# Performance work log

Measured on AMD Instinct MI355X. Metric: run time of the kernel, lower is better.

## Reference

```python
import jax, jax.numpy as jnp
import numpy as np

B, S, D = 16, 300, 768   # batch, hubert frames, embedding_dim
K = 512                  # vq codebook size
V = 5000                 # vocab size
H = 8                    # attention heads
NL = 4                   # encoder/decoder layers
L = 50                   # label length
EPS = 1e-5


def layer_norm(x, g, b):
    m = jnp.mean(x, axis=-1, keepdims=True)
    v = jnp.var(x, axis=-1, keepdims=True)
    return (x - m) * jax.lax.rsqrt(v + EPS) * g + b


def mha(q_in, kv_in, Wqkv, bqkv, Wo, bo, bias=None):
    # PyTorch nn.MultiheadAttention math (packed in_proj), batch_first
    Dm = q_in.shape[-1]
    hd = Dm // H
    Wq, Wk, Wv = jnp.split(Wqkv, 3, axis=0)
    bq, bk, bv = jnp.split(bqkv, 3, axis=0)
    q = (q_in @ Wq.T + bq).reshape(q_in.shape[0], -1, H, hd)
    k = (kv_in @ Wk.T + bk).reshape(kv_in.shape[0], -1, H, hd)
    v = (kv_in @ Wv.T + bv).reshape(kv_in.shape[0], -1, H, hd)
    scores = jnp.einsum('bthd,bshd->bhts', q, k) / jnp.sqrt(jnp.float32(hd))
    if bias is not None:
        scores = scores + bias
    a = jax.nn.softmax(scores, axis=-1)
    o = jnp.einsum('bhts,bshd->bthd', a, v).reshape(q_in.shape[0], -1, Dm)
    return o @ Wo.T + bo


def setup_inputs() -> dict:
    key = jax.random.key(0)
    ks = iter(jax.random.split(key, 64))
    f32 = jnp.float32
    def rn(shape, s=0.02):
        return jax.random.normal(next(ks), shape, f32) * s
    d = {}
    d['features'] = jax.random.normal(next(ks), (B, S, D), f32)
    d['labels'] = jax.random.randint(next(ks), (B, L), 1, V, jnp.int32)
    d['codebook'] = jax.random.normal(next(ks), (K, D), f32)   # normal_() init
    d['emb_layer'] = jax.random.normal(next(ks), (K, D), f32)  # nn.Embedding N(0,1)
    d['tok_emb'] = jax.random.normal(next(ks), (V, D), f32)
    d['fc_W'] = rn((V, D)); d['fc_b'] = jnp.zeros((V,), f32)
    for p in ['enc', 'dec_s', 'dec_c']:
        d[p + 'Wqkv' if p != 'enc' else 'enc_Wqkv'] = rn((NL, 3 * D, D))
    # rebuild cleanly with explicit names
    d['enc_Wqkv'] = rn((NL, 3 * D, D)); d['enc_bqkv'] = jnp.zeros((NL, 3 * D), f32)
    d['enc_Wo'] = rn((NL, D, D)); d['enc_bo'] = jnp.zeros((NL, D), f32)
    d['enc_ln1g'] = jnp.ones((NL, D), f32); d['enc_ln1b'] = jnp.zeros((NL, D), f32)
    d['enc_W1'] = rn((NL, 1536, D)); d['enc_b1'] = jnp.zeros((NL, 1536), f32)
    d['enc_W2'] = rn((NL, D, 1536)); d['enc_b2'] = jnp.zeros((NL, D), f32)
    d['enc_ln2g'] = jnp.ones((NL, D), f32); d['enc_ln2b'] = jnp.zeros((NL, D), f32)
    d['dec_sWqkv'] = rn((NL, 3 * D, D)); d['dec_sbqkv'] = jnp.zeros((NL, 3 * D), f32)
    d['dec_sWo'] = rn((NL, D, D)); d['dec_sbo'] = jnp.zeros((NL, D), f32)
    d['dec_cWqkv'] = rn((NL, 3 * D, D)); d['dec_cbqkv'] = jnp.zeros((NL, 3 * D), f32)
    d['dec_cWo'] = rn((NL, D, D)); d['dec_cbo'] = jnp.zeros((NL, D), f32)
    d['dec_ln1g'] = jnp.ones((NL, D), f32); d['dec_ln1b'] = jnp.zeros((NL, D), f32)
    d['dec_ln2g'] = jnp.ones((NL, D), f32); d['dec_ln2b'] = jnp.zeros((NL, D), f32)
    d['dec_ln3g'] = jnp.ones((NL, D), f32); d['dec_ln3b'] = jnp.zeros((NL, D), f32)
    d['dec_W1'] = rn((NL, 1536, D)); d['dec_b1'] = jnp.zeros((NL, 1536), f32)
    d['dec_W2'] = rn((NL, D, 1536)); d['dec_b2'] = jnp.zeros((NL, D), f32)
    return d


def forward(features, labels, codebook, emb_layer, tok_emb, fc_W, fc_b,
            enc_Wqkv, enc_bqkv, enc_Wo, enc_bo, enc_ln1g, enc_ln1b,
            enc_W1, enc_b1, enc_W2, enc_b2, enc_ln2g, enc_ln2b,
            dec_sWqkv, dec_sbqkv, dec_sWo, dec_sbo,
            dec_cWqkv, dec_cbqkv, dec_cWo, dec_cbo,
            dec_ln1g, dec_ln1b, dec_ln2g, dec_ln2b, dec_ln3g, dec_ln3b,
            dec_W1, dec_b1, dec_W2, dec_b2):
    # ---- VQ: pairwise distances + argmin + codebook gather ----
    x = features.reshape(-1, D)                                  # [N, D]
    dist = (jnp.sum(x * x, 1, keepdims=True)
            + jnp.sum(codebook * codebook, 1)
            - 2.0 * x @ codebook.T)                              # [N, K]
    idx = jnp.argmin(dist, axis=1)                               # [N]
    quantized = codebook[idx]                                    # one-hot @ codebook == gather
    # commitment loss (quantized is detached in e_latent_loss)
    vq_loss = 0.25 * jnp.mean((jax.lax.stop_gradient(quantized) - x) ** 2)
    # ---- encoder over embedding_layer lookup of the VQ indices ----
    h = emb_layer[idx].reshape(B, S, D)
    for i in range(NL):
        h = layer_norm(h + mha(h, h, enc_Wqkv[i], enc_bqkv[i], enc_Wo[i], enc_bo[i]),
                       enc_ln1g[i], enc_ln1b[i])
        ff = jax.nn.relu(h @ enc_W1[i].T + enc_b1[i]) @ enc_W2[i].T + enc_b2[i]
        h = layer_norm(h + ff, enc_ln2g[i], enc_ln2b[i])
    memory = h
    # ---- decoder (teacher forcing) ----
    dec_in = tok_emb[labels][:, :-1, :]                          # [B, L-1, D]
    target = labels[:, 1:]                                       # [B, L-1]
    T = L - 1
    causal = jnp.triu(jnp.ones((T, T), bool), 1)                 # tgt_mask
    kpm = (target == 0)[:, None, None, :]                        # tgt_key_padding_mask
    bias = jnp.where(causal[None, None] | kpm, jnp.float32(-1e9), jnp.float32(0.0))
    y = dec_in
    for i in range(NL):
        y = layer_norm(y + mha(y, y, dec_sWqkv[i], dec_sbqkv[i], dec_sWo[i], dec_sbo[i], bias),
                       dec_ln1g[i], dec_ln1b[i])
        y = layer_norm(y + mha(y, memory, dec_cWqkv[i], dec_cbqkv[i], dec_cWo[i], dec_cbo[i]),
                       dec_ln2g[i], dec_ln2b[i])
        ff = jax.nn.relu(y @ dec_W1[i].T + dec_b1[i]) @ dec_W2[i].T + dec_b2[i]
        y = layer_norm(y + ff, dec_ln3g[i], dec_ln3b[i])
    logits = y @ fc_W.T + fc_b                                   # [B, L-1, V]
    return logits, vq_loss, target


def reference(features, labels, codebook, emb_layer, tok_emb, fc_W, fc_b,
              enc_Wqkv, enc_bqkv, enc_Wo, enc_bo, enc_ln1g, enc_ln1b,
              enc_W1, enc_b1, enc_W2, enc_b2, enc_ln2g, enc_ln2b,
              dec_sWqkv, dec_sbqkv, dec_sWo, dec_sbo,
              dec_cWqkv, dec_cbqkv, dec_cWo, dec_cbo,
              dec_ln1g, dec_ln1b, dec_ln2g, dec_ln2b, dec_ln3g, dec_ln3b,
              dec_W1, dec_b1, dec_W2, dec_b2):
    return forward(features, labels, codebook, emb_layer, tok_emb, fc_W, fc_b,
                   enc_Wqkv, enc_bqkv, enc_Wo, enc_bo, enc_ln1g, enc_ln1b,
                   enc_W1, enc_b1, enc_W2, enc_b2, enc_ln2g, enc_ln2b,
                   dec_sWqkv, dec_sbqkv, dec_sWo, dec_sbo,
                   dec_cWqkv, dec_cbqkv, dec_cWo, dec_cbo,
                   dec_ln1g, dec_ln1b, dec_ln2g, dec_ln2b, dec_ln3g, dec_ln3b,
                   dec_W1, dec_b1, dec_W2, dec_b2)
```

## Files before the change

### kernel.cpp

```cpp
#include <hip/hip_runtime.h>
#include <hip/hip_bf16.h>

#define Bz   16
#define Sz   300
#define Dz   768
#define Kc   512
#define Vz   5000
#define Hh   8
#define HD   96
#define Lz   50
#define Tz   49
#define NTOK 4800
#define NDTOK 784

typedef short bf16x8 __attribute__((ext_vector_type(8)));
typedef float f32x4  __attribute__((ext_vector_type(4)));
typedef unsigned short us8 __attribute__((ext_vector_type(8)));

__device__ __forceinline__ unsigned short f2b(float f) {
    unsigned u = __float_as_uint(f);
    unsigned r = (u + 0x7fffu + ((u >> 16) & 1u)) >> 16;
    return (unsigned short)r;
}

__device__ __forceinline__ void glds16(const unsigned short* g, unsigned short* l) {
    __builtin_amdgcn_global_load_lds(
        (const __attribute__((address_space(1))) void*)g,
        (__attribute__((address_space(3))) void*)l, 16, 0, 0);
}

__global__ __launch_bounds__(256) void gemm_bf16_kernel(
    const unsigned short* __restrict__ A,
    const unsigned short* __restrict__ Bw,
    float* __restrict__ Cf,
    unsigned short* __restrict__ Cb,
    int ldc,
    const float* __restrict__ bias,
    const float* __restrict__ resid, int ldr,
    int relu, int M, int N, int Kd)
{
    __shared__ unsigned short As[128 * 32];
    __shared__ unsigned short Bs[128 * 32];
    const int tid  = threadIdx.x;
    const int wave = tid >> 6, lane = tid & 63;
    const int row0 = blockIdx.y * 128, col0 = blockIdx.x * 128;

    const int c0 = wave * 2;
    const int srow = lane >> 2;
    const int skcol = (lane & 3) * 8;
    int rA0 = row0 + c0 * 16 + srow;        if (rA0 > M - 1) rA0 = M - 1;
    int rA1 = row0 + (c0 + 1) * 16 + srow;  if (rA1 > M - 1) rA1 = M - 1;
    int rB0 = col0 + c0 * 16 + srow;        if (rB0 > N - 1) rB0 = N - 1;
    int rB1 = col0 + (c0 + 1) * 16 + srow;  if (rB1 > N - 1) rB1 = N - 1;
    const unsigned short* pA0 = A + (size_t)rA0 * Kd + skcol;
    const unsigned short* pA1 = A + (size_t)rA1 * Kd + skcol;
    const unsigned short* pB0 = Bw + (size_t)rB0 * Kd + skcol;
    const unsigned short* pB1 = Bw + (size_t)rB1 * Kd + skcol;
    unsigned short* lA0 = &As[c0 * 512];
    unsigned short* lA1 = &As[(c0 + 1) * 512];
    unsigned short* lB0 = &Bs[c0 * 512];
    unsigned short* lB1 = &Bs[(c0 + 1) * 512];

    const int wr = (wave >> 1) * 64, wc = (wave & 1) * 64;
    const int fr = lane & 15;
    const int kq = (lane >> 4) * 8;

    f32x4 acc[4][4];
    const f32x4 zero = { 0.f, 0.f, 0.f, 0.f };
#pragma unroll
    for (int i = 0; i < 4; ++i)
#pragma unroll
        for (int j = 0; j < 4; ++j) acc[i][j] = zero;

    for (int k0 = 0; k0 < Kd; k0 += 32) {
        __syncthreads();
        glds16(pA0 + k0, lA0);
        glds16(pA1 + k0, lA1);
        glds16(pB0 + k0, lB0);
        glds16(pB1 + k0, lB1);
        __syncthreads();

        bf16x8 af[4], bfr[4];
#pragma unroll
        for (int i = 0; i < 4; ++i)
            af[i] = *(const bf16x8*)(const void*)(&As[(wr + i * 16 + fr) * 32 + kq]);
#pragma unroll
        for (int j = 0; j < 4; ++j)
            bfr[j] = *(const bf16x8*)(const void*)(&Bs[(wc + j * 16 + fr) * 32 + kq]);
#pragma unroll
        for (int i = 0; i < 4; ++i)
#pragma unroll
            for (int j = 0; j < 4; ++j)
                acc[i][j] = __builtin_amdgcn_mfma_f32_16x16x32_bf16(
                    af[i], bfr[j], acc[i][j], 0, 0, 0);
    }

    const int rbase = row0 + wr + ((lane >> 4) << 2);
    const int cbase = col0 + wc + (lane & 15);
#pragma unroll
    for (int i = 0; i < 4; ++i) {
#pragma unroll
        for (int r = 0; r < 4; ++r) {
            int row = rbase + i * 16 + r;
            if (row >= M) continue;
#pragma unroll
            for (int j = 0; j < 4; ++j) {
                int col = cbase + j * 16;
                if (col >= N) continue;
                float v = acc[i][j][r];
                if (bias)  v += bias[col];
                if (resid) v += resid[(size_t)row * ldr + col];
                if (relu)  v = fmaxf(v, 0.f);
                if (Cf) Cf[(size_t)row * ldc + col] = v;
                if (Cb) Cb[(size_t)row * ldc + col] = f2b(v);
            }
        }
    }
}

__global__ __launch_bounds__(256) void gemm_bf16_64_kernel(
    const unsigned short* __restrict__ A,
    const unsigned short* __restrict__ Bw,
    float* __restrict__ Cf, unsigned short* __restrict__ Cb, int ldc,
    const float* __restrict__ bias,
    const float* __restrict__ resid, int ldr,
    int relu, int M, int N, int Kd)
{
    __shared__ unsigned short As[64 * 32];
    __shared__ unsigned short Bs[64 * 32];
    const int tid = threadIdx.x, wave = tid >> 6, lane = tid & 63;
    const int row0 = blockIdx.y * 64, col0 = blockIdx.x * 64;
    const int fr = lane & 15, quad = lane >> 4;

    const int sr = lane >> 2;
    const int sc = (lane & 3) * 8;
    int ra = row0 + wave * 16 + sr;  if (ra > M - 1) ra = M - 1;
    int rb = col0 + wave * 16 + sr;  if (rb > N - 1) rb = N - 1;
    const unsigned short* pA = A + (size_t)ra * Kd + sc;
    const unsigned short* pB = Bw + (size_t)rb * Kd + sc;
    unsigned short* lA = &As[wave * 512];
    unsigned short* lB = &Bs[wave * 512];

    f32x4 acc[4];
    const f32x4 zero = { 0.f, 0.f, 0.f, 0.f };
#pragma unroll
    for (int j = 0; j < 4; ++j) acc[j] = zero;

    for (int k0 = 0; k0 < Kd; k0 += 32) {
        __syncthreads();
        glds16(pA + k0, lA);
        glds16(pB + k0, lB);
        __syncthreads();
        bf16x8 a = *(const bf16x8*)(const void*)(&As[(wave * 16 + fr) * 32 + quad * 8]);
#pragma unroll
        for (int j = 0; j < 4; ++j) {
            bf16x8 b = *(const bf16x8*)(const void*)(&Bs[(j * 16 + fr) * 32 + quad * 8]);
            acc[j] = __builtin_amdgcn_mfma_f32_16x16x32_bf16(a, b, acc[j], 0, 0, 0);
        }
    }

    const int rbase = row0 + wave * 16 + quad * 4;
    const int cbase = col0 + fr;
#pragma unroll
    for (int r = 0; r < 4; ++r) {
        int row = rbase + r;
        if (row >= M) continue;
#pragma unroll
        for (int j = 0; j < 4; ++j) {
            int col = cbase + j * 16;
            if (col >= N) continue;
            float v = acc[j][r];
            if (bias)  v += bias[col];
            if (resid) v += resid[(size_t)row * ldr + col];
            if (relu)  v = fmaxf(v, 0.f);
            if (Cf) Cf[(size_t)row * ldc + col] = v;
            if (Cb) Cb[(size_t)row * ldc + col] = f2b(v);
        }
    }
}

__global__ __launch_bounds__(256) void vq_gemm_kernel(
    const float* __restrict__ A,
    const float* __restrict__ Bw,
    float* __restrict__ C)
{
    __shared__ float As[16][64];
    __shared__ float Bs[16][64];
    const int tid = threadIdx.x;
    const int row0 = blockIdx.y * 64, col0 = blockIdx.x * 64;
    const int tx = tid & 15, ty = tid >> 4;
    const int lm = tid >> 2, lk = (tid & 3) * 4;

    float acc[4][4];
#pragma unroll
    for (int i = 0; i < 4; ++i)
#pragma unroll
        for (int j = 0; j < 4; ++j) acc[i][j] = 0.f;

    const float* Ap = A + (size_t)(row0 + lm) * Dz + lk;
    const float* Bp = Bw + (size_t)(col0 + lm) * Dz + lk;

    for (int k0 = 0; k0 < Dz; k0 += 16) {
        float4 av = *(const float4*)(Ap + k0);
        float4 bv = *(const float4*)(Bp + k0);
        __syncthreads();
        As[lk + 0][lm] = av.x; As[lk + 1][lm] = av.y;
        As[lk + 2][lm] = av.z; As[lk + 3][lm] = av.w;
        Bs[lk + 0][lm] = bv.x; Bs[lk + 1][lm] = bv.y;
        Bs[lk + 2][lm] = bv.z; Bs[lk + 3][lm] = bv.w;
        __syncthreads();
#pragma unroll
        for (int kk = 0; kk < 16; ++kk) {
            float4 a4 = *(const float4*)&As[kk][ty * 4];
            float4 b4 = *(const float4*)&Bs[kk][tx * 4];
            float a[4] = { a4.x, a4.y, a4.z, a4.w };
            float b[4] = { b4.x, b4.y, b4.z, b4.w };
#pragma unroll
            for (int i = 0; i < 4; ++i)
#pragma unroll
                for (int j = 0; j < 4; ++j)
                    acc[i][j] = fmaf(a[i], b[j], acc[i][j]);
        }
    }

#pragma unroll
    for (int i = 0; i < 4; ++i)
#pragma unroll
        for (int j = 0; j < 4; ++j)
            C[(size_t)(row0 + ty * 4 + i) * Kc + col0 + tx * 4 + j] = acc[i][j];
}

#define SC_LD 324
#define P_LD  328
#define QK_LD 104
#define VT_LD 40

__global__ __launch_bounds__(256) void attn_mfma_kernel(
    const unsigned short* __restrict__ Qp, int qld, int qoff,
    const unsigned short* __restrict__ Kp, int kld, int koff,
    const unsigned short* __restrict__ Vp, int vld, int voff,
    unsigned short* __restrict__ Op,
    int Sq, int Sk, float scale, int causal,
    const int* __restrict__ lab)
{
    const int qt = blockIdx.x, h = blockIdx.y, b = blockIdx.z;
    const int q0 = qt * 32;
    __shared__ __align__(16) unsigned short Qs[32 * QK_LD];
    __shared__ __align__(16) unsigned short KVu[96 * VT_LD];
    __shared__ __align__(16) float Sc[32 * SC_LD];
    __shared__ __align__(16) unsigned short Pb[32 * P_LD];
    __shared__ float rinv[32];

    const int tid = threadIdx.x;
    const int wave = tid >> 6, lane = tid & 63;
    const int fr = lane & 15, quad = lane >> 4;
    const int nst = (Sk + 31) / 32;
    const int cmax = nst * 32;

    for (int e = tid; e < 384; e += 256) {
        int r = e / 12, c8 = (e % 12) * 8;
        int gq = q0 + r; if (gq >= Sq) gq = Sq - 1;
        us8 v = *(const us8*)(Qp + (size_t)(b * Sq + gq) * qld + qoff + h * HD + c8);
        *(us8*)(&Qs[r * QK_LD + c8]) = v;
    }

    const int mi = wave & 1;
    const int sw = wave >> 1;
    for (int it = 0; it < nst; ++it) {
        int s0 = it * 32;
        __syncthreads();
        for (int e = tid; e < 384; e += 256) {
            int r = e / 12, c8 = (e % 12) * 8;
            int gk = s0 + r; if (gk >= Sk) gk = Sk - 1;
            us8 v = *(const us8*)(Kp + (size_t)(b * Sk + gk) * kld + koff + h * HD + c8);
            *(us8*)(&KVu[r * QK_LD + c8]) = v;
        }
        __syncthreads();
        f32x4 acc = { 0.f, 0.f, 0.f, 0.f };
#pragma unroll
        for (int kk = 0; kk < 3; ++kk) {
            bf16x8 a = *(const bf16x8*)(const void*)(&Qs[(mi * 16 + fr) * QK_LD + kk * 32 + quad * 8]);
            bf16x8 bb = *(const bf16x8*)(const void*)(&KVu[(sw * 16 + fr) * QK_LD + kk * 32 + quad * 8]);
            acc = __builtin_amdgcn_mfma_f32_16x16x32_bf16(a, bb, acc, 0, 0, 0);
        }
        float* dst = &Sc[(mi * 16 + quad * 4) * SC_LD + s0 + sw * 16 + fr];
#pragma unroll
        for (int r = 0; r < 4; ++r) dst[r * SC_LD] = acc[r];
    }
    __syncthreads();

    {
        const int r = tid >> 3, sub = tid & 7;
        const int gq = q0 + r;
        float mx = -3e38f;
        for (int c = sub; c < cmax; c += 8) {
            float v = Sc[r * SC_LD + c];
            bool ok = (c < Sk);
            if (causal && c > gq) ok = false;
            if (ok && lab && lab[b * Lz + c + 1] == 0) ok = false;
            v = ok ? v * scale : -3e38f;
            Sc[r * SC_LD + c] = v;
            mx = fmaxf(mx, v);
        }
#pragma unroll
        for (int off = 4; off > 0; off >>= 1) mx = fmaxf(mx, __shfl_xor(mx, off));
        float sum = 0.f;
        for (int c = sub; c < cmax; c += 8) {
            float p = __expf(Sc[r * SC_LD + c] - mx);
            sum += p;
            Pb[r * P_LD + c] = f2b(p);
        }
#pragma unroll
        for (int off = 4; off > 0; off >>= 1) sum += __shfl_xor(sum, off);
        if (sub == 0) rinv[r] = 1.f / sum;
    }

    const int nbase = (wave >> 1) * 3;
    f32x4 oacc[3];
#pragma unroll
    for (int t = 0; t < 3; ++t) oacc[t] = (f32x4){ 0.f, 0.f, 0.f, 0.f };

    for (int it = 0; it < nst; ++it) {
        int s0 = it * 32;
        __syncthreads();
        for (int e = tid; e < 384; e += 256) {
            int r = e / 12, c8 = (e % 12) * 8;
            int gk = s0 + r; if (gk >= Sk) gk = Sk - 1;
            us8 v = *(const us8*)(Vp + (size_t)(b * Sk + gk) * vld + voff + h * HD + c8);
            const int f = ((c8 >> 3) & 3) << 3;
            const int rx = r ^ f;
#pragma unroll
            for (int j = 0; j < 8; ++j)
                KVu[(c8 + j) * VT_LD + rx] = v[j];
        }
        __syncthreads();
        bf16x8 a = *(const bf16x8*)(const void*)(&Pb[(mi * 16 + fr) * P_LD + s0 + quad * 8]);
#pragma unroll
        for (int t = 0; t < 3; ++t) {
            const int dcol = (nbase + t) * 16 + fr;
            const int f2 = ((dcol >> 3) & 3) << 3;
            bf16x8 bv = *(const bf16x8*)(const void*)(&KVu[dcol * VT_LD + ((quad * 8) ^ f2)]);
            oacc[t] = __builtin_amdgcn_mfma_f32_16x16x32_bf16(a, bv, oacc[t], 0, 0, 0);
        }
    }

#pragma unroll
    for (int t = 0; t < 3; ++t) {
#pragma unroll
        for (int r = 0; r < 4; ++r) {
            int lrow = mi * 16 + quad * 4 + r;
            int grow = q0 + lrow;
            if (grow >= Sq) continue;
            int col = h * HD + (nbase + t) * 16 + fr;
            Op[(size_t)(b * Sq + grow) * Dz + col] = f2b(oacc[t][r] * rinv[lrow]);
        }
    }
}

__global__ __launch_bounds__(256) void ln_kernel(
    const float* __restrict__ X, float* __restrict__ Y,
    unsigned short* __restrict__ Ybf,
    const float* __restrict__ g, const float* __restrict__ bb)
{
    const int n = blockIdx.x;
    const int tid = threadIdx.x;
    const float* x = X + (size_t)n * Dz;
    float v0 = x[tid], v1 = x[tid + 256], v2 = x[tid + 512];
    float s = v0 + v1 + v2;
    float q = v0 * v0 + v1 * v1 + v2 * v2;
#pragma unroll
    for (int off = 32; off > 0; off >>= 1) {
        s += __shfl_down(s, off);
        q += __shfl_down(q, off);
    }
    __shared__ float sbuf[4], qbuf[4];
    __shared__ float mv[2];
    int wid = tid >> 6;
    if ((tid & 63) == 0) { sbuf[wid] = s; qbuf[wid] = q; }
    __syncthreads();
    if (tid == 0) {
        float ts = sbuf[0] + sbuf[1] + sbuf[2] + sbuf[3];
        float tq = qbuf[0] + qbuf[1] + qbuf[2] + qbuf[3];
        float mean = ts * (1.f / 768.f);
        float var = tq * (1.f / 768.f) - mean * mean;
        mv[0] = mean;
        mv[1] = rsqrtf(var + 1e-5f);
    }
    __syncthreads();
    float mean = mv[0], inv = mv[1];
    float* y = Y + (size_t)n * Dz;
    float r0 = (v0 - mean) * inv * g[tid]       + bb[tid];
    float r1 = (v1 - mean) * inv * g[tid + 256] + bb[tid + 256];
    float r2 = (v2 - mean) * inv * g[tid + 512] + bb[tid + 512];
    y[tid] = r0; y[tid + 256] = r1; y[tid + 512] = r2;
    if (Ybf) {
        unsigned short* yb = Ybf + (size_t)n * Dz;
        yb[tid] = f2b(r0); yb[tid + 256] = f2b(r1); yb[tid + 512] = f2b(r2);
    }
}

__global__ __launch_bounds__(256) void sumsq_kernel(
    const float* __restrict__ cb, float* __restrict__ out)
{
    const int c = blockIdx.x, tid = threadIdx.x;
    const float* x = cb + (size_t)c * Dz;
    float v0 = x[tid], v1 = x[tid + 256], v2 = x[tid + 512];
    float q = v0 * v0 + v1 * v1 + v2 * v2;
#pragma unroll
    for (int off = 32; off > 0; off >>= 1) q += __shfl_down(q, off);
    __shared__ float qbuf[4];
    int wid = tid >> 6;
    if ((tid & 63) == 0) qbuf[wid] = q;
    __syncthreads();
    if (tid == 0) out[c] = qbuf[0] + qbuf[1] + qbuf[2] + qbuf[3];
}

__global__ __launch_bounds__(256) void vq_post_kernel(
    const float* __restrict__ dots, const float* __restrict__ sumc2,
    const float* __restrict__ feats, const float* __restrict__ codebook,
    const float* __restrict__ emb, float* __restrict__ H,
    unsigned short* __restrict__ Hbf,
    float* __restrict__ loss)
{
    const int n = blockIdx.x, tid = threadIdx.x;
    float best = 3.4e38f; int bi = 0;
    for (int c = tid; c < Kc; c += 256) {
        float dct = sumc2[c] - 2.f * dots[(size_t)n * Kc + c];
        if (dct < best) { best = dct; bi = c; }
    }
#pragma unroll
    for (int off = 32; off > 0; off >>= 1) {
        float ov = __shfl_down(best, off);
        int   oi = __shfl_down(bi, off);
        if (ov < best || (ov == best && oi < bi)) { best = ov; bi = oi; }
    }
    __shared__ float vb[4]; __shared__ int ib[4];
    __shared__ int bidx;
    int wid = tid >> 6;
    if ((tid & 63) == 0) { vb[wid] = best; ib[wid] = bi; }
    __syncthreads();
    if (tid == 0) {
        float v = vb[0]; int i = ib[0];
        for (int w = 1; w < 4; ++w)
            if (vb[w] < v || (vb[w] == v && ib[w] < i)) { v = vb[w]; i = ib[w]; }
        bidx = i;
    }
    __syncthreads();
    const int c = bidx;
    float part = 0.f;
    for (int d = tid; d < Dz; d += 256) {
        float xv = feats[(size_t)n * Dz + d];
        float cv = codebook[(size_t)c * Dz + d];
        float df = cv - xv;
        part += df * df;
        float ev = emb[(size_t)c * Dz + d];
        H[(size_t)n * Dz + d] = ev;
        Hbf[(size_t)n * Dz + d] = f2b(ev);
    }
#pragma unroll
    for (int off = 32; off > 0; off >>= 1) part += __shfl_down(part, off);
    __shared__ float pb[4];
    if ((tid & 63) == 0) pb[wid] = part;
    __syncthreads();
    if (tid == 0) atomicAdd(loss, pb[0] + pb[1] + pb[2] + pb[3]);
}

__global__ __launch_bounds__(256) void dec_embed_kernel(
    const int* __restrict__ labels, const float* __restrict__ tok,
    float* __restrict__ Y, unsigned short* __restrict__ Ybf,
    float* __restrict__ tgt)
{
    const int t = blockIdx.x;
    const int b = t / Tz, pos = t % Tz;
    const int lab = labels[b * Lz + pos];
    const int tid = threadIdx.x;
    const float* src = tok + (size_t)lab * Dz;
    float* dst = Y + (size_t)t * Dz;
    unsigned short* dbf = Ybf + (size_t)t * Dz;
    float a = src[tid], b1 = src[tid + 256], c = src[tid + 512];
    dst[tid] = a; dst[tid + 256] = b1; dst[tid + 512] = c;
    dbf[tid] = f2b(a); dbf[tid + 256] = f2b(b1); dbf[tid + 512] = f2b(c);
    if (tid == 0) tgt[t] = (float)labels[b * Lz + pos + 1];
}

__global__ void zero_loss_kernel(float* loss) { *loss = 0.f; }

__global__ void finalize_kernel(const float* loss, float* out)
{
    out[0] = loss[0] * (0.25f / (float)(NTOK * Dz));
}

__global__ __launch_bounds__(256) void conv6_kernel(
    const float* p0, int n0, const float* p1, int n1,
    const float* p2, int n2, const float* p3, int n3,
    const float* p4, int n4, const float* p5, int n5,
    unsigned short* __restrict__ dst)
{
    const int total = n0 + n1 + n2 + n3 + n4 + n5;
    for (int i = blockIdx.x * blockDim.x + threadIdx.x; i < total;
         i += gridDim.x * blockDim.x) {
        int j = i; const float* p;
        if (j < n0) { p = p0; }
        else { j -= n0;
            if (j < n1) { p = p1; }
            else { j -= n1;
                if (j < n2) { p = p2; }
                else { j -= n2;
                    if (j < n3) { p = p3; }
                    else { j -= n3;
                        if (j < n4) { p = p4; }
                        else { j -= n4; p = p5; }
                    }
                }
            }
        }
        dst[i] = f2b(p[j]);
    }
}

extern "C" void kernel_launch(void* const* d_in, const int* in_sizes, int n_in,
                              void* d_out, int out_size, void* d_ws, size_t ws_size,
                              hipStream_t stream)
{
    bool sig = (n_in > 8 && in_sizes[8] == 9216);
    int I_eWqkv, I_ebqkv, I_eWo, I_ebo, I_eln1g, I_eln1b, I_eW1, I_eb1, I_eW2, I_eb2,
        I_eln2g, I_eln2b, I_sWqkv, I_sbqkv, I_sWo, I_sbo, I_cWqkv, I_cbqkv, I_cWo,
        I_cbo, I_dln1g, I_dln1b, I_dln2g, I_dln2b, I_dln3g, I_dln3b, I_dW1, I_db1,
        I_dW2, I_db2;
    if (sig) {
        I_eWqkv = 7; I_ebqkv = 8; I_eWo = 9; I_ebo = 10; I_eln1g = 11; I_eln1b = 12;
        I_eW1 = 13; I_eb1 = 14; I_eW2 = 15; I_eb2 = 16; I_eln2g = 17; I_eln2b = 18;
        I_sWqkv = 19; I_sbqkv = 20; I_sWo = 21; I_sbo = 22;
        I_cWqkv = 23; I_cbqkv = 24; I_cWo = 25; I_cbo = 26;
        I_dln1g = 27; I_dln1b = 28; I_dln2g = 29; I_dln2b = 30; I_dln3g = 31; I_dln3b = 32;
        I_dW1 = 33; I_db1 = 34; I_dW2 = 35; I_db2 = 36;
    } else {
        I_eWqkv = 7; I_sWqkv = 8; I_cWqkv = 9;
        I_ebqkv = 10; I_eWo = 11; I_ebo = 12; I_eln1g = 13; I_eln1b = 14;
        I_eW1 = 15; I_eb1 = 16; I_eW2 = 17; I_eb2 = 18; I_eln2g = 19; I_eln2b = 20;
        I_sbqkv = 21; I_sWo = 22; I_sbo = 23;
        I_cbqkv = 24; I_cWo = 25; I_cbo = 26;
        I_dln1g = 27; I_dln1b = 28; I_dln2g = 29; I_dln2b = 30; I_dln3g = 31; I_dln3b = 32;
        I_dW1 = 33; I_db1 = 34; I_dW2 = 35; I_db2 = 36;
    }

    const float* feats = (const float*)d_in[0];
    const int*   labels = (const int*)d_in[1];
    const float* cb    = (const float*)d_in[2];
    const float* emb   = (const float*)d_in[3];
    const float* tok   = (const float*)d_in[4];
    const float* fcW   = (const float*)d_in[5];
    const float* fcb   = (const float*)d_in[6];
    const float* eWqkv = (const float*)d_in[I_eWqkv];
    const float* ebqkv = (const float*)d_in[I_ebqkv];
    const float* eWo   = (const float*)d_in[I_eWo];
    const float* ebo   = (const float*)d_in[I_ebo];
    const float* eln1g = (const float*)d_in[I_eln1g];
    const float* eln1b = (const float*)d_in[I_eln1b];
    const float* eW1   = (const float*)d_in[I_eW1];
    const float* eb1   = (const float*)d_in[I_eb1];
    const float* eW2   = (const float*)d_in[I_eW2];
    const float* eb2   = (const float*)d_in[I_eb2];
    const float* eln2g = (const float*)d_in[I_eln2g];
    const float* eln2b = (const float*)d_in[I_eln2b];
    const float* sWqkv = (const float*)d_in[I_sWqkv];
    const float* sbqkv = (const float*)d_in[I_sbqkv];
    const float* sWo   = (const float*)d_in[I_sWo];
    const float* sbo   = (const float*)d_in[I_sbo];
    const float* cWqkv = (const float*)d_in[I_cWqkv];
    const float* cbqkv = (const float*)d_in[I_cbqkv];
    const float* cWo   = (const float*)d_in[I_cWo];
    const float* cbo   = (const float*)d_in[I_cbo];
    const float* dln1g = (const float*)d_in[I_dln1g];
    const float* dln1b = (const float*)d_in[I_dln1b];
    const float* dln2g = (const float*)d_in[I_dln2g];
    const float* dln2b = (const float*)d_in[I_dln2b];
    const float* dln3g = (const float*)d_in[I_dln3g];
    const float* dln3b = (const float*)d_in[I_dln3b];
    const float* dW1   = (const float*)d_in[I_dW1];
    const float* db1   = (const float*)d_in[I_db1];
    const float* dW2   = (const float*)d_in[I_dW2];
    const float* db2   = (const float*)d_in[I_db2];

    float* ws    = (float*)d_ws;
    float* sumc2 = ws;
    float* loss  = ws + 512;
    float* Hb    = ws + 1024;
    float* T1    = ws + 3687424;
    float* dots  = ws + 7373824;
    float* Yb    = T1;
    float* T1d   = T1 + 602112;

    unsigned short* bfbase = (unsigned short*)(ws + 9831424);
    unsigned short* Hb_bf  = bfbase;
    unsigned short* ATT_bf = bfbase + 3686400;
    unsigned short* FF_bf  = bfbase + 7372800;
    unsigned short* Yb_bf  = bfbase + 14745600;
    unsigned short* Wbuf   = bfbase + 15347712;
    unsigned short* QKV_bf = bfbase + 22425600;
    unsigned short* QKVd_bf = QKV_bf;
    unsigned short* Qc_bf   = QKV_bf + 1806336;
    unsigned short* CKV_bf  = QKV_bf + 2408448;

    float* outF = (float*)d_out;

    auto gemmb = [&](const unsigned short* A, const unsigned short* W,
                     float* Cf, unsigned short* Cb, int ldc,
                     const float* bias, const float* resid, int ldr,
                     int relu, int M, int N, int Kd) {
        dim3 g((N + 127) / 128, (M + 127) / 128);
        gemm_bf16_kernel<<<g, 256, 0, stream>>>(A, W, Cf, Cb, ldc, bias, resid, ldr,
                                                relu, M, N, Kd);
    };
    auto gemmb64 = [&](const unsigned short* A, const unsigned short* W,
                       float* Cf, unsigned short* Cb, int ldc,
                       const float* bias, const float* resid, int ldr,
                       int relu, int M, int N, int Kd) {
        dim3 g((N + 63) / 64, (M + 63) / 64);
        gemm_bf16_64_kernel<<<g, 256, 0, stream>>>(A, W, Cf, Cb, ldc, bias, resid, ldr,
                                                   relu, M, N, Kd);
    };

    const float scale = 0.1020620726159658f;
    const float* Z = nullptr;

    zero_loss_kernel<<<1, 1, 0, stream>>>(loss);
    sumsq_kernel<<<Kc, 256, 0, stream>>>(cb, sumc2);
    vq_gemm_kernel<<<dim3(8, 75), 256, 0, stream>>>(feats, cb, dots);
    vq_post_kernel<<<NTOK, 256, 0, stream>>>(dots, sumc2, feats, cb, emb, Hb, Hb_bf, loss);
    finalize_kernel<<<1, 1, 0, stream>>>(loss, outF + 3920000);

    const int W_QKV = 2304 * 768, W_O = 768 * 768, W_F1 = 1536 * 768, W_F2 = 768 * 1536;
    for (int i = 0; i < 4; ++i) {
        conv6_kernel<<<1024, 256, 0, stream>>>(
            eWqkv + (size_t)i * W_QKV, W_QKV,
            eWo   + (size_t)i * W_O,   W_O,
            eW1   + (size_t)i * W_F1,  W_F1,
            eW2   + (size_t)i * W_F2,  W_F2,
            Z, 0, Z, 0, Wbuf);
        unsigned short* bWqkv = Wbuf;
        unsigned short* bWo   = Wbuf + W_QKV;
        unsigned short* bW1   = Wbuf + W_QKV + W_O;
        unsigned short* bW2   = Wbuf + W_QKV + W_O + W_F1;

        gemmb(Hb_bf, bWqkv, nullptr, QKV_bf, 2304, ebqkv + i * 2304, Z, 0, 0, NTOK, 2304, Dz);
        attn_mfma_kernel<<<dim3(10, Hh, Bz), 256, 0, stream>>>(
            QKV_bf, 2304, 0, QKV_bf, 2304, 768, QKV_bf, 2304, 1536, ATT_bf,
            Sz, Sz, scale, 0, nullptr);
        gemmb(ATT_bf, bWo, T1, nullptr, Dz, ebo + i * Dz, Hb, Dz, 0, NTOK, Dz, Dz);
        ln_kernel<<<NTOK, 256, 0, stream>>>(T1, Hb, Hb_bf, eln1g + i * Dz, eln1b + i * Dz);
        gemmb(Hb_bf, bW1, nullptr, FF_bf, 1536, eb1 + i * 1536, Z, 0, 1, NTOK, 1536, Dz);
        gemmb(FF_bf, bW2, T1, nullptr, Dz, eb2 + i * Dz, Hb, Dz, 0, NTOK, Dz, 1536);
        ln_kernel<<<NTOK, 256, 0, stream>>>(T1, Hb, Hb_bf, eln2g + i * Dz, eln2b + i * Dz);
    }

    dec_embed_kernel<<<NDTOK, 256, 0, stream>>>(labels, tok, Yb, Yb_bf, outF + 3920001);
    for (int i = 0; i < 4; ++i) {
        conv6_kernel<<<1024, 256, 0, stream>>>(
            sWqkv + (size_t)i * W_QKV, W_QKV,
            sWo   + (size_t)i * W_O,   W_O,
            cWqkv + (size_t)i * W_QKV, W_QKV,
            cWo   + (size_t)i * W_O,   W_O,
            dW1   + (size_t)i * W_F1,  W_F1,
            dW2   + (size_t)i * W_F2,  W_F2, Wbuf);
        unsigned short* bsWqkv = Wbuf;
        unsigned short* bsWo   = Wbuf + W_QKV;
        unsigned short* bcWqkv = Wbuf + W_QKV + W_O;
        unsigned short* bcWo   = Wbuf + 2 * W_QKV + W_O;
        unsigned short* bW1    = Wbuf + 2 * W_QKV + 2 * W_O;
        unsigned short* bW2    = Wbuf + 2 * W_QKV + 2 * W_O + W_F1;

        gemmb64(Yb_bf, bsWqkv, nullptr, QKVd_bf, 2304, sbqkv + i * 2304, Z, 0, 0, NDTOK, 2304, Dz);
        attn_mfma_kernel<<<dim3(2, Hh, Bz), 256, 0, stream>>>(
            QKVd_bf, 2304, 0, QKVd_bf, 2304, 768, QKVd_bf, 2304, 1536, ATT_bf,
            Tz, Tz, scale, 1, labels);
        gemmb64(ATT_bf, bsWo, T1d, nullptr, Dz, sbo + i * Dz, Yb, Dz, 0, NDTOK, Dz, Dz);
        ln_kernel<<<NDTOK, 256, 0, stream>>>(T1d, Yb, Yb_bf, dln1g + i * Dz, dln1b + i * Dz);
        gemmb64(Yb_bf, bcWqkv, nullptr, Qc_bf, Dz, cbqkv + i * 2304, Z, 0, 0, NDTOK, Dz, Dz);
        gemmb(Hb_bf, bcWqkv + (size_t)768 * 768, nullptr, CKV_bf, 1536,
              cbqkv + i * 2304 + 768, Z, 0, 0, NTOK, 1536, Dz);
        attn_mfma_kernel<<<dim3(2, Hh, Bz), 256, 0, stream>>>(
            Qc_bf, 768, 0, CKV_bf, 1536, 0, CKV_bf, 1536, 768, ATT_bf,
            Tz, Sz, scale, 0, nullptr);
        gemmb64(ATT_bf, bcWo, T1d, nullptr, Dz, cbo + i * Dz, Yb, Dz, 0, NDTOK, Dz, Dz);
        ln_kernel<<<NDTOK, 256, 0, stream>>>(T1d, Yb, Yb_bf, dln2g + i * Dz, dln2b + i * Dz);
        gemmb64(Yb_bf, bW1, nullptr, FF_bf, 1536, db1 + i * 1536, Z, 0, 1, NDTOK, 1536, Dz);
        gemmb64(FF_bf, bW2, T1d, nullptr, Dz, db2 + i * Dz, Yb, Dz, 0, NDTOK, Dz, 1536);
        ln_kernel<<<NDTOK, 256, 0, stream>>>(T1d, Yb, Yb_bf, dln3g + i * Dz, dln3b + i * Dz);
    }

    conv6_kernel<<<1024, 256, 0, stream>>>(fcW, Vz * Dz, Z, 0, Z, 0, Z, 0, Z, 0, Z, 0, Wbuf);
    gemmb64(Yb_bf, Wbuf, outF, nullptr, Vz, fcb, Z, 0, 0, NDTOK, Vz, Dz);
}
```

Baseline: 2.486 ms.

## Use split-bf16 MFMA for VQ distances, smaller decoder GEMM tiles, vectorized weight conversion

The FP32 SIMT VQ distance GEMM is replaced by splitting features and codebook into bf16 hi/lo parts laid out along a tripled K dimension, then running the bf16 MFMA GEMM (hi*hi + hi*lo + lo*hi). Decoder GEMMs move from 64x64 to 32x64 tiles to launch more blocks for the small M=784 problem. The weight fp32-to-bf16 conversion kernel is vectorized with float4 loads and launched with twice the blocks, and the loss zeroing is folded into the sumsq kernel. The split VQ path adds two conversion passes and drops the lo*lo term, which may perturb argmin ties.

Result: faster. 2.341 ms (-5.8%).

```diff
diff --git a/kernel.cpp b/kernel.cpp
--- a/kernel.cpp
+++ b/kernel.cpp
@@ -21,6 +21,9 @@
     unsigned u = __float_as_uint(f);
     unsigned r = (u + 0x7fffu + ((u >> 16) & 1u)) >> 16;
     return (unsigned short)r;
+}
+__device__ __forceinline__ float b2f(unsigned short h) {
+    return __uint_as_float(((unsigned)h) << 16);
 }
 
 __device__ __forceinline__ void glds16(const unsigned short* g, unsigned short* l) {
@@ -118,7 +121,7 @@
     }
 }
 
-__global__ __launch_bounds__(256) void gemm_bf16_64_kernel(
+__global__ __launch_bounds__(256) void gemm_bf16_32_kernel(
     const unsigned short* __restrict__ A,
     const unsigned short* __restrict__ Bw,
     float* __restrict__ Cf, unsigned short* __restrict__ Cb, int ldc,
@@ -126,50 +129,69 @@
     const float* __restrict__ resid, int ldr,
     int relu, int M, int N, int Kd)
 {
-    __shared__ unsigned short As[64 * 32];
+    __shared__ unsigned short As[32 * 32];
     __shared__ unsigned short Bs[64 * 32];
     const int tid = threadIdx.x, wave = tid >> 6, lane = tid & 63;
-    const int row0 = blockIdx.y * 64, col0 = blockIdx.x * 64;
+    const int row0 = blockIdx.y * 32, col0 = blockIdx.x * 64;
     const int fr = lane & 15, quad = lane >> 4;
-
     const int sr = lane >> 2;
     const int sc = (lane & 3) * 8;
-    int ra = row0 + wave * 16 + sr;  if (ra > M - 1) ra = M - 1;
-    int rb = col0 + wave * 16 + sr;  if (rb > N - 1) rb = N - 1;
-    const unsigned short* pA = A + (size_t)ra * Kd + sc;
-    const unsigned short* pB = Bw + (size_t)rb * Kd + sc;
-    unsigned short* lA = &As[wave * 512];
-    unsigned short* lB = &Bs[wave * 512];
-
-    f32x4 acc[4];
-    const f32x4 zero = { 0.f, 0.f, 0.f, 0.f };
-#pragma unroll
-    for (int j = 0; j < 4; ++j) acc[j] = zero;
+
+    const unsigned short* pA = nullptr;
+    const unsigned short* pB0 = nullptr;
+    const unsigned short* pB1 = nullptr;
+    unsigned short* lA = nullptr;
+    unsigned short* lB0 = nullptr;
+    unsigned short* lB1 = nullptr;
+    if (wave < 2) {
+        int ra = row0 + wave * 16 + sr; if (ra > M - 1) ra = M - 1;
+        pA = A + (size_t)ra * Kd + sc;
+        lA = &As[wave * 512];
+    } else {
+        int w2 = wave - 2;
+        int rb0 = col0 + w2 * 16 + sr;       if (rb0 > N - 1) rb0 = N - 1;
+        int rb1 = col0 + 32 + w2 * 16 + sr;  if (rb1 > N - 1) rb1 = N - 1;
+        pB0 = Bw + (size_t)rb0 * Kd + sc;
+        pB1 = Bw + (size_t)rb1 * Kd + sc;
+        lB0 = &Bs[w2 * 512];
+        lB1 = &Bs[1024 + w2 * 512];
+    }
+
+    f32x4 acc[2];
+    acc[0] = (f32x4){ 0.f, 0.f, 0.f, 0.f };
+    acc[1] = (f32x4){ 0.f, 0.f, 0.f, 0.f };
+
+    const int mrow = (wave & 1) * 16 + fr;
+    const int ng = (wave >> 1) * 32;
 
     for (int k0 = 0; k0 < Kd; k0 += 32) {
         __syncthreads();
-        glds16(pA + k0, lA);
-        glds16(pB + k0, lB);
-        __syncthreads();
-        bf16x8 a = *(const bf16x8*)(const void*)(&As[(wave * 16 + fr) * 32 + quad * 8]);
-#pragma unroll
-        for (int j = 0; j < 4; ++j) {
-            bf16x8 b = *(const bf16x8*)(const void*)(&Bs[(j * 16 + fr) * 32 + quad * 8]);
-            acc[j] = __builtin_amdgcn_mfma_f32_16x16x32_bf16(a, b, acc[j], 0, 0, 0);
-        }
-    }
-
-    const int rbase = row0 + wave * 16 + quad * 4;
-    const int cbase = col0 + fr;
+        if (wave < 2) {
+            glds16(pA + k0, lA);
+        } else {
+            glds16(pB0 + k0, lB0);
+            glds16(pB1 + k0, lB1);
+        }
+        __syncthreads();
+        bf16x8 a = *(const bf16x8*)(const void*)(&As[mrow * 32 + quad * 8]);
+#pragma unroll
+        for (int t = 0; t < 2; ++t) {
+            bf16x8 b = *(const bf16x8*)(const void*)(&Bs[(ng + t * 16 + fr) * 32 + quad * 8]);
+            acc[t] = __builtin_amdgcn_mfma_f32_16x16x32_bf16(a, b, acc[t], 0, 0, 0);
+        }
+    }
+
+    const int rbase = row0 + (wave & 1) * 16 + quad * 4;
+    const int cbase = col0 + ng + fr;
 #pragma unroll
     for (int r = 0; r < 4; ++r) {
         int row = rbase + r;
         if (row >= M) continue;
 #pragma unroll
-        for (int j = 0; j < 4; ++j) {
-            int col = cbase + j * 16;
+        for (int t = 0; t < 2; ++t) {
+            int col = cbase + t * 16;
             if (col >= N) continue;
-            float v = acc[j][r];
+            float v = acc[t][r];
             if (bias)  v += bias[col];
             if (resid) v += resid[(size_t)row * ldr + col];
             if (relu)  v = fmaxf(v, 0.f);
@@ -179,55 +201,19 @@
     }
 }
 
-__global__ __launch_bounds__(256) void vq_gemm_kernel(
-    const float* __restrict__ A,
-    const float* __restrict__ Bw,
-    float* __restrict__ C)
-{
-    __shared__ float As[16][64];
-    __shared__ float Bs[16][64];
-    const int tid = threadIdx.x;
-    const int row0 = blockIdx.y * 64, col0 = blockIdx.x * 64;
-    const int tx = tid & 15, ty = tid >> 4;
-    const int lm = tid >> 2, lk = (tid & 3) * 4;
-
-    float acc[4][4];
-#pragma unroll
-    for (int i = 0; i < 4; ++i)
-#pragma unroll
-        for (int j = 0; j < 4; ++j) acc[i][j] = 0.f;
-
-    const float* Ap = A + (size_t)(row0 + lm) * Dz + lk;
-    const float* Bp = Bw + (size_t)(col0 + lm) * Dz + lk;
-
-    for (int k0 = 0; k0 < Dz; k0 += 16) {
-        float4 av = *(const float4*)(Ap + k0);
-        float4 bv = *(const float4*)(Bp + k0);
-        __syncthreads();
-        As[lk + 0][lm] = av.x; As[lk + 1][lm] = av.y;
-        As[lk + 2][lm] = av.z; As[lk + 3][lm] = av.w;
-        Bs[lk + 0][lm] = bv.x; Bs[lk + 1][lm] = bv.y;
-        Bs[lk + 2][lm] = bv.z; Bs[lk + 3][lm] = bv.w;
-        __syncthreads();
-#pragma unroll
-        for (int kk = 0; kk < 16; ++kk) {
-            float4 a4 = *(const float4*)&As[kk][ty * 4];
-            float4 b4 = *(const float4*)&Bs[kk][tx * 4];
-            float a[4] = { a4.x, a4.y, a4.z, a4.w };
-            float b[4] = { b4.x, b4.y, b4.z, b4.w };
-#pragma unroll
-            for (int i = 0; i < 4; ++i)
-#pragma unroll
-                for (int j = 0; j < 4; ++j)
-                    acc[i][j] = fmaf(a[i], b[j], acc[i][j]);
-        }
-    }
-
-#pragma unroll
-    for (int i = 0; i < 4; ++i)
-#pragma unroll
-        for (int j = 0; j < 4; ++j)
-            C[(size_t)(row0 + ty * 4 + i) * Kc + col0 + tx * 4 + j] = acc[i][j];
+__global__ __launch_bounds__(256) void vq_split_kernel(
+    const float* __restrict__ src, unsigned short* __restrict__ dst,
+    int nrows, int pattern)
+{
+    int i = blockIdx.x * 256 + threadIdx.x;
+    if (i >= nrows * Dz) return;
+    int r = i / Dz, c = i % Dz;
+    float x = src[i];
+    unsigned short h = f2b(x);
+    unsigned short l = f2b(x - b2f(h));
+    unsigned short* d = dst + (size_t)r * 2304 + c;
+    if (pattern == 0) { d[0] = h; d[768] = h; d[1536] = l; }
+    else              { d[0] = h; d[768] = l; d[1536] = h; }
 }
 
 #define SC_LD 324
@@ -400,9 +386,10 @@
 }
 
 __global__ __launch_bounds__(256) void sumsq_kernel(
-    const float* __restrict__ cb, float* __restrict__ out)
+    const float* __restrict__ cb, float* __restrict__ out, float* __restrict__ loss)
 {
     const int c = blockIdx.x, tid = threadIdx.x;
+    if (c == 0 && tid == 0) *loss = 0.f;
     const float* x = cb + (size_t)c * Dz;
     float v0 = x[tid], v1 = x[tid + 256], v2 = x[tid + 512];
     float q = v0 * v0 + v1 * v1 + v2 * v2;
@@ -483,8 +470,6 @@
     if (tid == 0) tgt[t] = (float)labels[b * Lz + pos + 1];
 }
 
-__global__ void zero_loss_kernel(float* loss) { *loss = 0.f; }
-
 __global__ void finalize_kernel(const float* loss, float* out)
 {
     out[0] = loss[0] * (0.25f / (float)(NTOK * Dz));
@@ -496,25 +481,30 @@
     const float* p4, int n4, const float* p5, int n5,
     unsigned short* __restrict__ dst)
 {
-    const int total = n0 + n1 + n2 + n3 + n4 + n5;
-    for (int i = blockIdx.x * blockDim.x + threadIdx.x; i < total;
+    const int m0 = n0 >> 2, m1 = n1 >> 2, m2 = n2 >> 2,
+              m3 = n3 >> 2, m4 = n4 >> 2, m5 = n5 >> 2;
+    const int total4 = m0 + m1 + m2 + m3 + m4 + m5;
+    for (int i = blockIdx.x * blockDim.x + threadIdx.x; i < total4;
          i += gridDim.x * blockDim.x) {
         int j = i; const float* p;
-        if (j < n0) { p = p0; }
-        else { j -= n0;
-            if (j < n1) { p = p1; }
-            else { j -= n1;
-                if (j < n2) { p = p2; }
-                else { j -= n2;
-                    if (j < n3) { p = p3; }
-                    else { j -= n3;
-                        if (j < n4) { p = p4; }
-                        else { j -= n4; p = p5; }
+        if (j < m0) { p = p0; }
+        else { j -= m0;
+            if (j < m1) { p = p1; }
+            else { j -= m1;
+                if (j < m2) { p = p2; }
+                else { j -= m2;
+                    if (j < m3) { p = p3; }
+                    else { j -= m3;
+                        if (j < m4) { p = p4; }
+                        else { j -= m4; p = p5; }
                     }
                 }
             }
         }
-        dst[i] = f2b(p[j]);
+        float4 v = ((const float4*)p)[j];
+        ushort4 o;
+        o.x = f2b(v.x); o.y = f2b(v.y); o.z = f2b(v.z); o.w = f2b(v.w);
+        ((ushort4*)dst)[i] = o;
     }
 }
 
@@ -601,6 +591,8 @@
     unsigned short* QKVd_bf = QKV_bf;
     unsigned short* Qc_bf   = QKV_bf + 1806336;
     unsigned short* CKV_bf  = QKV_bf + 2408448;
+    unsigned short* Asplit  = QKV_bf;
+    unsigned short* Bsplit  = FF_bf;
 
     float* outF = (float*)d_out;
 
@@ -612,27 +604,28 @@
         gemm_bf16_kernel<<<g, 256, 0, stream>>>(A, W, Cf, Cb, ldc, bias, resid, ldr,
                                                 relu, M, N, Kd);
     };
-    auto gemmb64 = [&](const unsigned short* A, const unsigned short* W,
+    auto gemmb32 = [&](const unsigned short* A, const unsigned short* W,
                        float* Cf, unsigned short* Cb, int ldc,
                        const float* bias, const float* resid, int ldr,
                        int relu, int M, int N, int Kd) {
-        dim3 g((N + 63) / 64, (M + 63) / 64);
-        gemm_bf16_64_kernel<<<g, 256, 0, stream>>>(A, W, Cf, Cb, ldc, bias, resid, ldr,
+        dim3 g((N + 63) / 64, (M + 31) / 32);
+        gemm_bf16_32_kernel<<<g, 256, 0, stream>>>(A, W, Cf, Cb, ldc, bias, resid, ldr,
                                                    relu, M, N, Kd);
     };
 
     const float scale = 0.1020620726159658f;
     const float* Z = nullptr;
 
-    zero_loss_kernel<<<1, 1, 0, stream>>>(loss);
-    sumsq_kernel<<<Kc, 256, 0, stream>>>(cb, sumc2);
-    vq_gemm_kernel<<<dim3(8, 75), 256, 0, stream>>>(feats, cb, dots);
+    sumsq_kernel<<<Kc, 256, 0, stream>>>(cb, sumc2, loss);
+    vq_split_kernel<<<(NTOK * Dz + 255) / 256, 256, 0, stream>>>(feats, Asplit, NTOK, 0);
+    vq_split_kernel<<<(Kc * Dz + 255) / 256, 256, 0, stream>>>(cb, Bsplit, Kc, 1);
+    gemmb32(Asplit, Bsplit, dots, nullptr, Kc, Z, Z, 0, 0, NTOK, Kc, 2304);
     vq_post_kernel<<<NTOK, 256, 0, stream>>>(dots, sumc2, feats, cb, emb, Hb, Hb_bf, loss);
     finalize_kernel<<<1, 1, 0, stream>>>(loss, outF + 3920000);
 
     const int W_QKV = 2304 * 768, W_O = 768 * 768, W_F1 = 1536 * 768, W_F2 = 768 * 1536;
     for (int i = 0; i < 4; ++i) {
-        conv6_kernel<<<1024, 256, 0, stream>>>(
+        conv6_kernel<<<2048, 256, 0, stream>>>(
             eWqkv + (size_t)i * W_QKV, W_QKV,
             eWo   + (size_t)i * W_O,   W_O,
             eW1   + (size_t)i * W_F1,  W_F1,
@@ -656,7 +649,7 @@
 
     dec_embed_kernel<<<NDTOK, 256, 0, stream>>>(labels, tok, Yb, Yb_bf, outF + 3920001);
     for (int i = 0; i < 4; ++i) {
-        conv6_kernel<<<1024, 256, 0, stream>>>(
+        conv6_kernel<<<2048, 256, 0, stream>>>(
             sWqkv + (size_t)i * W_QKV, W_QKV,
             sWo   + (size_t)i * W_O,   W_O,
             cWqkv + (size_t)i * W_QKV, W_QKV,
@@ -670,25 +663,25 @@
         unsigned short* bW1    = Wbuf + 2 * W_QKV + 2 * W_O;
         unsigned short* bW2    = Wbuf + 2 * W_QKV + 2 * W_O + W_F1;
 
-        gemmb64(Yb_bf, bsWqkv, nullptr, QKVd_bf, 2304, sbqkv + i * 2304, Z, 0, 0, NDTOK, 2304, Dz);
+        gemmb32(Yb_bf, bsWqkv, nullptr, QKVd_bf, 2304, sbqkv + i * 2304, Z, 0, 0, NDTOK, 2304, Dz);
         attn_mfma_kernel<<<dim3(2, Hh, Bz), 256, 0, stream>>>(
             QKVd_bf, 2304, 0, QKVd_bf, 2304, 768, QKVd_bf, 2304, 1536, ATT_bf,
             Tz, Tz, scale, 1, labels);
-        gemmb64(ATT_bf, bsWo, T1d, nullptr, Dz, sbo + i * Dz, Yb, Dz, 0, NDTOK, Dz, Dz);
+        gemmb32(ATT_bf, bsWo, T1d, nullptr, Dz, sbo + i * Dz, Yb, Dz, 0, NDTOK, Dz, Dz);
         ln_kernel<<<NDTOK, 256, 0, stream>>>(T1d, Yb, Yb_bf, dln1g + i * Dz, dln1b + i * Dz);
-        gemmb64(Yb_bf, bcWqkv, nullptr, Qc_bf, Dz, cbqkv + i * 2304, Z, 0, 0, NDTOK, Dz, Dz);
+        gemmb32(Yb_bf, bcWqkv, nullptr, Qc_bf, Dz, cbqkv + i * 2304, Z, 0, 0, NDTOK, Dz, Dz);
         gemmb(Hb_bf, bcWqkv + (size_t)768 * 768, nullptr, CKV_bf, 1536,
               cbqkv + i * 2304 + 768, Z, 0, 0, NTOK, 1536, Dz);
         attn_mfma_kernel<<<dim3(2, Hh, Bz), 256, 0, stream>>>(
             Qc_bf, 768, 0, CKV_bf, 1536, 0, CKV_bf, 1536, 768, ATT_bf,
             Tz, Sz, scale, 0, nullptr);
-        gemmb64(ATT_bf, bcWo, T1d, nullptr, Dz, cbo + i * Dz, Yb, Dz, 0, NDTOK, Dz, Dz);
+        gemmb32(ATT_bf, bcWo, T1d, nullptr, Dz, cbo + i * Dz, Yb, Dz, 0, NDTOK, Dz, Dz);
         ln_kernel<<<NDTOK, 256, 0, stream>>>(T1d, Yb, Yb_bf, dln2g + i * Dz, dln2b + i * Dz);
-        gemmb64(Yb_bf, bW1, nullptr, FF_bf, 1536, db1 + i * 1536, Z, 0, 1, NDTOK, 1536, Dz);
-        gemmb64(FF_bf, bW2, T1d, nullptr, Dz, db2 + i * Dz, Yb, Dz, 0, NDTOK, Dz, 1536);
+        gemmb32(Yb_bf, bW1, nullptr, FF_bf, 1536, db1 + i * 1536, Z, 0, 1, NDTOK, 1536, Dz);
+        gemmb32(FF_bf, bW2, T1d, nullptr, Dz, db2 + i * Dz, Yb, Dz, 0, NDTOK, Dz, 1536);
         ln_kernel<<<NDTOK, 256, 0, stream>>>(T1d, Yb, Yb_bf, dln3g + i * Dz, dln3b + i * Dz);
     }
 
-    conv6_kernel<<<1024, 256, 0, stream>>>(fcW, Vz * Dz, Z, 0, Z, 0, Z, 0, Z, 0, Z, 0, Wbuf);
-    gemmb64(Yb_bf, Wbuf, outF, nullptr, Vz, fcb, Z, 0, 0, NDTOK, Vz, Dz);
-}
+    conv6_kernel<<<2048, 256, 0, stream>>>(fcW, Vz * Dz, Z, 0, Z, 0, Z, 0, Z, 0, Z, 0, Wbuf);
+    gemmb32(Yb_bf, Wbuf, outF, nullptr, Vz, fcb, Z, 0, 0, NDTOK, Vz, Dz);
+}
```
